# Kernel optimization log

Hardware: AMD Instinct MI355X
Metric: run time of the kernel (lower is better)

## Reference

```python
import jax, jax.numpy as jnp
import numpy as np

N = 50000      # nodes
R = 4          # relations
E = 1600000    # edges per relation
IN = 256       # in_feats
H = 256        # h_feats
C = 16         # num_classes


def setup_inputs() -> dict:
    key = jax.random.key(0)
    ks = jax.random.split(key, 8)
    X = jax.random.normal(ks[0], (N, IN), jnp.float32)
    edge_index = jax.random.randint(ks[1], (R, 2, E), 0, N, dtype=jnp.int32)
    W1 = jax.random.normal(ks[2], (R, IN, H), jnp.float32) * (1.0 / np.sqrt(IN))
    W2 = jax.random.normal(ks[3], (R, H, H), jnp.float32) * (1.0 / np.sqrt(H))
    att_q = jax.random.normal(ks[4], (H,), jnp.float32) * (1.0 / np.sqrt(H))
    tau = jnp.asarray(2.0, jnp.float32)
    W_out = jax.random.normal(ks[5], (H, C), jnp.float32) * (1.0 / np.sqrt(H))
    b_out = jnp.zeros((C,), jnp.float32)
    return {"X": X, "edge_index": edge_index, "W1": W1, "W2": W2,
            "att_q": att_q, "tau": tau, "W_out": W_out, "b_out": b_out}


def _sym_norm_spmm(edge, feat):
    """out = D^{-1/2} A D^{-1/2} @ feat for one relation, edge: [2,E]."""
    row, col = edge[0], edge[1]
    ones = jnp.ones(edge.shape[1], feat.dtype)
    deg_r = jax.ops.segment_sum(ones, row, num_segments=N)
    deg_c = jax.ops.segment_sum(ones, col, num_segments=N)
    dinv_r = jax.lax.rsqrt(jnp.maximum(deg_r, 1.0))
    dinv_c = jax.lax.rsqrt(jnp.maximum(deg_c, 1.0))
    w = dinv_r[row] * dinv_c[col]                      # [E]
    msg = w[:, None] * feat[col]                       # gather + scale
    return jax.ops.segment_sum(msg, row, num_segments=N)  # [N, F]


def _rel_layer(edge_index, feat, W):
    # vmapped over relations: ReLU(A_r feat W_r) -> [R, N, H]
    def one(edge, Wr):
        return jax.nn.relu(_sym_norm_spmm(edge, feat) @ Wr)
    return jax.vmap(one)(edge_index, W)


def reference(X, edge_index, W1, W2, att_q, tau, W_out, b_out):
    # Layer 1: mean over relations (eval mode: no dropout)
    H1 = _rel_layer(edge_index, X, W1)        # [R, N, H]
    h1 = H1.mean(axis=0)                      # [N, H]
    # Layer 2 with relation attention
    H2 = _rel_layer(edge_index, h1, W2)       # [R, N, H]
    scores = jnp.einsum('rnh,h->nr', H2, att_q)
    tau_c = jnp.clip(tau, 0.5, 5.0)
    alpha = jax.nn.softmax(scores / tau_c, axis=1)   # [N, R]
    h2_att = jnp.einsum('nr,rnh->nh', alpha, H2)
    h2 = H2.mean(axis=0) + h2_att             # residual fusion
    logits = h2 @ W_out + b_out               # [N, C]
    return logits, alpha
```

## Files before the change

### kernel.cpp

```cpp
#include <hip/hip_runtime.h>
#include <hip/hip_bf16.h>
#include <stdint.h>

#define NODES 50000
#define RELS  4
#define EDGES 1600000
#define FEAT  256
#define NCLS  16
#define MPAD  50048
#define RPS   50016
#define SCHUNK 1024
#define NSBLK  49
#define NCHUNK 64
#define CHUNKE 25000
#define NB     782

typedef __attribute__((ext_vector_type(8))) short short8;
typedef __attribute__((ext_vector_type(8))) unsigned short u16x8;
typedef __attribute__((ext_vector_type(4))) float f32x4;

static __device__ __forceinline__ float bf2f(unsigned short u) {
    return __uint_as_float(((unsigned int)u) << 16);
}
static __device__ __forceinline__ unsigned short f2bf(float f) {
    unsigned int x = __float_as_uint(f);
    unsigned int r = x + 0x7fffu + ((x >> 16) & 1u);
    return (unsigned short)(r >> 16);
}


__global__ __launch_bounds__(256)
void k_bhist2(const int* __restrict__ edges, unsigned* __restrict__ partR,
              unsigned* __restrict__ partC) {
    int chunk = blockIdx.x, rel = blockIdx.y, t = threadIdx.x;
    const int* rows = edges + (size_t)rel * 2 * EDGES + (size_t)chunk * CHUNKE;
    const int* cols = rows + EDGES;
    __shared__ unsigned hR[NB];
    __shared__ unsigned hC[NB];
    for (int i = t; i < NB; i += 256) { hR[i] = 0; hC[i] = 0; }
    __syncthreads();
    for (int e = t; e < CHUNKE; e += 256) {
        atomicAdd(&hR[((unsigned)rows[e]) >> 6], 1u);
        atomicAdd(&hC[((unsigned)cols[e]) >> 6], 1u);
    }
    __syncthreads();
    unsigned* pR = partR + ((size_t)rel * NCHUNK + chunk) * NB;
    unsigned* pC = partC + ((size_t)rel * NCHUNK + chunk) * NB;
    for (int i = t; i < NB; i += 256) { pR[i] = hR[i]; pC[i] = hC[i]; }
}

__global__ __launch_bounds__(256)
void k_bscan(const unsigned* __restrict__ part, unsigned* __restrict__ off,
             unsigned* __restrict__ bbase) {
    int rel = blockIdx.x, t = threadIdx.x;
    const int BPT = 4;
    int b0 = t * BPT;
    unsigned s = 0;
#pragma unroll
    for (int j = 0; j < BPT; ++j) {
        int b = b0 + j;
        unsigned x = 0;
        if (b < NB)
            for (int c = 0; c < NCHUNK; ++c)
                x += part[((size_t)rel * NCHUNK + c) * NB + b];
        s += x;
    }
    __shared__ unsigned sh[256];
    sh[t] = s;
    __syncthreads();
    for (int o = 1; o < 256; o <<= 1) {
        unsigned u = (t >= o) ? sh[t - o] : 0;
        __syncthreads();
        sh[t] += u;
        __syncthreads();
    }
    unsigned base = sh[t] - s;
#pragma unroll
    for (int j = 0; j < BPT; ++j) {
        int b = b0 + j;
        if (b < NB) {
            bbase[rel * (NB + 1) + b] = base;
            unsigned acc = base;
            for (int c = 0; c < NCHUNK; ++c) {
                size_t o2 = ((size_t)rel * NCHUNK + c) * NB + b;
                off[o2] = acc;
                acc += part[o2];
            }
            base = acc;
        }
    }
    if (t == 255) bbase[rel * (NB + 1) + NB] = sh[255];
}

__global__ __launch_bounds__(256)
void k_scat2(const int* __restrict__ edges, const unsigned* __restrict__ offR,
             const unsigned* __restrict__ offC, int2* __restrict__ ebuf,
             int* __restrict__ cbuf) {
    int chunk = blockIdx.x, rel = blockIdx.y, t = threadIdx.x;
    const int* rows = edges + (size_t)rel * 2 * EDGES + (size_t)chunk * CHUNKE;
    const int* cols = rows + EDGES;
    __shared__ unsigned curR[NB];
    __shared__ unsigned curC[NB];
    const unsigned* pR = offR + ((size_t)rel * NCHUNK + chunk) * NB;
    const unsigned* pC = offC + ((size_t)rel * NCHUNK + chunk) * NB;
    for (int i = t; i < NB; i += 256) { curR[i] = pR[i]; curC[i] = pC[i]; }
    __syncthreads();
    int2* eb = ebuf + (size_t)rel * EDGES;
    int*  cb = cbuf + (size_t)rel * EDGES;
    for (int e = t; e < CHUNKE; e += 256) {
        int r = rows[e], c = cols[e];
        unsigned pr = atomicAdd(&curR[((unsigned)r) >> 6], 1u);
        eb[pr] = make_int2(r, c);
        unsigned pc = atomicAdd(&curC[((unsigned)c) >> 6], 1u);
        cb[pc] = c;
    }
}

__global__ __launch_bounds__(256)
void k_countR(const int2* __restrict__ ebuf, const unsigned* __restrict__ bbase,
              int* __restrict__ deg_row) {
    int b = blockIdx.x, rel = blockIdx.y, t = threadIdx.x;
    unsigned s = bbase[rel * (NB + 1) + b], e = bbase[rel * (NB + 1) + b + 1];
    __shared__ unsigned cnt[64];
    if (t < 64) cnt[t] = 0;
    __syncthreads();
    const int2* eb = ebuf + (size_t)rel * EDGES;
    for (unsigned i = s + t; i < e; i += 256) atomicAdd(&cnt[eb[i].x & 63], 1u);
    __syncthreads();
    int base = b * 64;
    if (t < 64 && base + t < NODES) deg_row[(size_t)rel * NODES + base + t] = (int)cnt[t];
}

__global__ __launch_bounds__(256)
void k_countC(const int* __restrict__ cbuf, const unsigned* __restrict__ bbase,
              int* __restrict__ deg_col) {
    int b = blockIdx.x, rel = blockIdx.y, t = threadIdx.x;
    unsigned s = bbase[rel * (NB + 1) + b], e = bbase[rel * (NB + 1) + b + 1];
    __shared__ unsigned cnt[64];
    if (t < 64) cnt[t] = 0;
    __syncthreads();
    const int* cb = cbuf + (size_t)rel * EDGES;
    for (unsigned i = s + t; i < e; i += 256) atomicAdd(&cnt[cb[i] & 63], 1u);
    __syncthreads();
    int base = b * 64;
    if (t < 64 && base + t < NODES) deg_col[(size_t)rel * NODES + base + t] = (int)cnt[t];
}

__global__ void k_dinv(const int* __restrict__ deg_row, const int* __restrict__ deg_col,
                       float* dinv_row, float* dinv_col) {
    int idx = blockIdx.x * blockDim.x + threadIdx.x;
    if (idx >= RELS * NODES) return;
    int dr = deg_row[idx]; if (dr < 1) dr = 1;
    int dc = deg_col[idx]; if (dc < 1) dc = 1;
    dinv_row[idx] = rsqrtf((float)dr);
    dinv_col[idx] = rsqrtf((float)dc);
}

__global__ __launch_bounds__(256)
void k_scanA(const int* __restrict__ deg, int* __restrict__ tmp, int* __restrict__ btot) {
    int r = blockIdx.y, blk = blockIdx.x, t = threadIdx.x;
    int i0 = blk * SCHUNK + t * 4;
    const int* d = deg + (size_t)r * NODES;
    int4 v = make_int4(0, 0, 0, 0);
    if (i0 + 3 < NODES) v = *(const int4*)(d + i0);
    else if (i0 < NODES) {
        v.x = d[i0];
        if (i0 + 1 < NODES) v.y = d[i0 + 1];
        if (i0 + 2 < NODES) v.z = d[i0 + 2];
    }
    int s = v.x + v.y + v.z + v.w;
    __shared__ int sh[256];
    sh[t] = s;
    __syncthreads();
    for (int off = 1; off < 256; off <<= 1) {
        int u = (t >= off) ? sh[t - off] : 0;
        __syncthreads();
        sh[t] += u;
        __syncthreads();
    }
    int excl = sh[t] - s;
    int4 o;
    o.x = excl; o.y = excl + v.x; o.z = o.y + v.y; o.w = o.z + v.z;
    int* tp = tmp + (size_t)r * NODES;
    if (i0 + 3 < NODES) *(int4*)(tp + i0) = o;
    else if (i0 < NODES) {
        tp[i0] = o.x;
        if (i0 + 1 < NODES) tp[i0 + 1] = o.y;
        if (i0 + 2 < NODES) tp[i0 + 2] = o.z;
    }
    if (t == 255) btot[r * 64 + blk] = sh[255];
}

__global__ void k_scanB(int* __restrict__ btot, int* __restrict__ row_ptr) {
    int r = blockIdx.x;
    if (threadIdx.x != 0) return;
    int acc = 0;
    for (int b = 0; b < NSBLK; ++b) {
        int v = btot[r * 64 + b];
        btot[r * 64 + b] = acc;
        acc += v;
    }
    row_ptr[r * RPS + NODES] = acc;
}

__global__ __launch_bounds__(256)
void k_scanC(const int* __restrict__ tmp, const int* __restrict__ btot,
             int* __restrict__ row_ptr) {
    int r = blockIdx.y, blk = blockIdx.x, t = threadIdx.x;
    int i0 = blk * SCHUNK + t * 4;
    int off = btot[r * 64 + blk];
    const int* tp = tmp + (size_t)r * NODES;
    int* rp = row_ptr + (size_t)r * RPS;
    if (i0 + 3 < NODES) {
        int4 v = *(const int4*)(tp + i0);
        rp[i0] = v.x + off; rp[i0 + 1] = v.y + off;
        rp[i0 + 2] = v.z + off; rp[i0 + 3] = v.w + off;
    } else if (i0 < NODES) {
        for (int j = 0; j < 4 && i0 + j < NODES; ++j)
            rp[i0 + j] = tp[i0 + j] + off;
    }
}

__global__ __launch_bounds__(256)
void k_place(const int2* __restrict__ ebuf, const unsigned* __restrict__ bbase,
             const int* __restrict__ row_ptr, int* __restrict__ csr_col) {
    int b = blockIdx.x, rel = blockIdx.y, t = threadIdx.x;
    unsigned s = bbase[rel * (NB + 1) + b], e = bbase[rel * (NB + 1) + b + 1];
    __shared__ int cur[64];
    int base = b * 64;
    const int* rp = row_ptr + (size_t)rel * RPS;
    if (t < 64) cur[t] = (base + t < NODES) ? rp[base + t] : 0;
    __syncthreads();
    const int2* eb = ebuf + (size_t)rel * EDGES;
    int* cc = csr_col + (size_t)rel * EDGES;
    for (unsigned i = s + t; i < e; i += 256) {
        int2 ec = eb[i];
        int pos = atomicAdd(&cur[ec.x - base], 1);
        cc[pos] = ec.y;
    }
}


__global__ __launch_bounds__(256)
void k_f2bf8(const float* __restrict__ src, unsigned short* __restrict__ dst, int count8) {
    int i = blockIdx.x * 256 + threadIdx.x;
    if (i >= count8) return;
    const float* s = src + (size_t)i * 8;
    float4 a = *(const float4*)s;
    float4 b = *(const float4*)(s + 4);
    u16x8 v;
    v[0] = f2bf(a.x); v[1] = f2bf(a.y); v[2] = f2bf(a.z); v[3] = f2bf(a.w);
    v[4] = f2bf(b.x); v[5] = f2bf(b.y); v[6] = f2bf(b.z); v[7] = f2bf(b.w);
    *(u16x8*)(dst + (size_t)i * 8) = v;
}

__global__ void k_wt2(const float* __restrict__ W1, const float* __restrict__ W2,
                      unsigned short* __restrict__ W1t, unsigned short* __restrict__ W2t) {
    int idx = blockIdx.x * blockDim.x + threadIdx.x;
    const int half = RELS * FEAT * FEAT;
    if (idx >= 2 * half) return;
    const float* W = (idx < half) ? W1 : W2;
    unsigned short* Wt = (idx < half) ? W1t : W2t;
    int id = (idx < half) ? idx : idx - half;
    int r = id >> 16;
    int rem = id & 65535;
    int n = rem >> 8;
    int k = rem & 255;
    Wt[id] = f2bf(W[(size_t)r * FEAT * FEAT + (size_t)k * FEAT + n]);
}


__global__ __launch_bounds__(256)
void k_spmm(const unsigned short* __restrict__ feat, const int* __restrict__ row_ptr,
            const int* __restrict__ csr_col, const float* __restrict__ dinv_row,
            const float* __restrict__ dinv_col, unsigned short* __restrict__ aggbase,
            int slice_off) {
    int rel = blockIdx.y;
    unsigned short* aggbf = aggbase + (size_t)(rel + slice_off) * (size_t)MPAD * FEAT;
    int wave = (blockIdx.x * blockDim.x + threadIdx.x) >> 6;
    int lane = threadIdx.x & 63;
    if (wave >= NODES) return;
    int row = wave;
    int half = lane >> 5;
    int l32  = lane & 31;
    int start = row_ptr[rel * RPS + row];
    int end   = row_ptr[rel * RPS + row + 1];
    const int* cols = csr_col + (size_t)rel * EDGES;
    const float* dc = dinv_col + rel * NODES;
    const unsigned short* fb = feat + l32 * 8;
    float acc[8] = {0.f, 0.f, 0.f, 0.f, 0.f, 0.f, 0.f, 0.f};
    int j = start + half;
    for (; j + 2 < end; j += 4) {
        int c0 = cols[j];
        int c1 = cols[j + 2];
        float w0 = dc[c0];
        float w1 = dc[c1];
        u16x8 u0 = *(const u16x8*)(fb + (size_t)c0 * FEAT);
        u16x8 u1 = *(const u16x8*)(fb + (size_t)c1 * FEAT);
#pragma unroll
        for (int i = 0; i < 8; ++i) acc[i] += w0 * bf2f(u0[i]);
#pragma unroll
        for (int i = 0; i < 8; ++i) acc[i] += w1 * bf2f(u1[i]);
    }
    if (j < end) {
        int c0 = cols[j];
        float w0 = dc[c0];
        u16x8 u0 = *(const u16x8*)(fb + (size_t)c0 * FEAT);
#pragma unroll
        for (int i = 0; i < 8; ++i) acc[i] += w0 * bf2f(u0[i]);
    }
#pragma unroll
    for (int i = 0; i < 8; ++i) acc[i] += __shfl_down(acc[i], 32, 64);
    if (half == 0) {
        float dr = dinv_row[rel * NODES + row];
        u16x8 o;
#pragma unroll
        for (int i = 0; i < 8; ++i) o[i] = f2bf(acc[i] * dr);
        *(u16x8*)(aggbf + (size_t)row * FEAT + l32 * 8) = o;
    }
}


__global__ __launch_bounds__(256)
void k_gemm1(const unsigned short* __restrict__ Abase, const unsigned short* __restrict__ Wt,
             unsigned short* __restrict__ h1bf) {
    __shared__ __align__(16) unsigned short As[128 * 64];
    __shared__ __align__(16) unsigned short Bs[128 * 64];
    int tid = threadIdx.x;
    int wave = tid >> 6, lane = tid & 63;
    int quad = lane >> 4, l16 = lane & 15;
    int wm = (wave & 1) * 64, wn = (wave >> 1) * 64;
    int row0 = blockIdx.x * 128, n0 = blockIdx.y * 128;

    f32x4 hacc[4][4];
#pragma unroll
    for (int mi = 0; mi < 4; ++mi)
#pragma unroll
        for (int ni = 0; ni < 4; ++ni)
            hacc[mi][ni] = (f32x4){0.f, 0.f, 0.f, 0.f};

    for (int r = 0; r < RELS; ++r) {
        const unsigned short* A  = Abase + (size_t)r * MPAD * FEAT;
        const unsigned short* Bt = Wt + (size_t)r * FEAT * FEAT;
        f32x4 acc[4][4];
#pragma unroll
        for (int mi = 0; mi < 4; ++mi)
#pragma unroll
            for (int ni = 0; ni < 4; ++ni)
                acc[mi][ni] = (f32x4){0.f, 0.f, 0.f, 0.f};

        for (int k0 = 0; k0 < FEAT; k0 += 64) {
#pragma unroll
            for (int issue = 0; issue < 4; ++issue) {
                int flat = issue * 256 + tid;
                int row = flat >> 3;
                int gr = flat & 7;
                int sg = gr ^ (row & 7);
                *(uint4*)&As[flat * 8] = *(const uint4*)(A + (size_t)(row0 + row) * FEAT + k0 + sg * 8);
                *(uint4*)&Bs[flat * 8] = *(const uint4*)(Bt + (size_t)(n0 + row) * FEAT + k0 + sg * 8);
            }
            __syncthreads();
#pragma unroll
            for (int ks = 0; ks < 2; ++ks) {
                int g = ks * 4 + quad;
                short8 af[4], bfr[4];
#pragma unroll
                for (int mi = 0; mi < 4; ++mi) {
                    int m = wm + mi * 16 + l16;
                    af[mi] = *(const short8*)&As[m * 64 + ((g ^ (m & 7)) << 3)];
                }
#pragma unroll
                for (int ni = 0; ni < 4; ++ni) {
                    int n = wn + ni * 16 + l16;
                    bfr[ni] = *(const short8*)&Bs[n * 64 + ((g ^ (n & 7)) << 3)];
                }
#pragma unroll
                for (int mi = 0; mi < 4; ++mi)
#pragma unroll
                    for (int ni = 0; ni < 4; ++ni)
                        acc[mi][ni] = __builtin_amdgcn_mfma_f32_16x16x32_bf16(af[mi], bfr[ni], acc[mi][ni], 0, 0, 0);
            }
            __syncthreads();
        }
#pragma unroll
        for (int mi = 0; mi < 4; ++mi)
#pragma unroll
            for (int ni = 0; ni < 4; ++ni)
#pragma unroll
                for (int i = 0; i < 4; ++i) {
                    float v = acc[mi][ni][i];
                    hacc[mi][ni][i] += 0.25f * (v > 0.f ? v : 0.f);
                }
    }

#pragma unroll
    for (int mi = 0; mi < 4; ++mi)
#pragma unroll
        for (int ni = 0; ni < 4; ++ni) {
            int col = n0 + wn + ni * 16 + l16;
#pragma unroll
            for (int i = 0; i < 4; ++i) {
                int row = row0 + wm + mi * 16 + quad * 4 + i;
                if (row < NODES) h1bf[(size_t)row * FEAT + col] = f2bf(hacc[mi][ni][i]);
            }
        }
}

__global__ __launch_bounds__(256)
void k_gemm2z(const unsigned short* __restrict__ aggbase, const unsigned short* __restrict__ Wtb,
              unsigned short* __restrict__ o0, unsigned short* __restrict__ o1,
              unsigned short* __restrict__ o2, unsigned short* __restrict__ o3) {
    __shared__ __align__(16) unsigned short As[128 * 64];
    __shared__ __align__(16) unsigned short Bs[128 * 64];
    int rz = blockIdx.z;
    const unsigned short* A  = aggbase + (size_t)(rz + 1) * MPAD * FEAT;
    const unsigned short* Bt = Wtb + (size_t)rz * FEAT * FEAT;
    unsigned short* H2 = (rz == 0) ? o0 : (rz == 1) ? o1 : (rz == 2) ? o2 : o3;

    int tid = threadIdx.x;
    int wave = tid >> 6, lane = tid & 63;
    int quad = lane >> 4, l16 = lane & 15;
    int wm = (wave & 1) * 64, wn = (wave >> 1) * 64;
    int row0 = blockIdx.x * 128, n0 = blockIdx.y * 128;

    f32x4 acc[4][4];
#pragma unroll
    for (int mi = 0; mi < 4; ++mi)
#pragma unroll
        for (int ni = 0; ni < 4; ++ni)
            acc[mi][ni] = (f32x4){0.f, 0.f, 0.f, 0.f};

    for (int k0 = 0; k0 < FEAT; k0 += 64) {
#pragma unroll
        for (int issue = 0; issue < 4; ++issue) {
            int flat = issue * 256 + tid;
            int row = flat >> 3;
            int gr = flat & 7;
            int sg = gr ^ (row & 7);
            *(uint4*)&As[flat * 8] = *(const uint4*)(A + (size_t)(row0 + row) * FEAT + k0 + sg * 8);
            *(uint4*)&Bs[flat * 8] = *(const uint4*)(Bt + (size_t)(n0 + row) * FEAT + k0 + sg * 8);
        }
        __syncthreads();
#pragma unroll
        for (int ks = 0; ks < 2; ++ks) {
            int g = ks * 4 + quad;
            short8 af[4], bfr[4];
#pragma unroll
            for (int mi = 0; mi < 4; ++mi) {
                int m = wm + mi * 16 + l16;
                af[mi] = *(const short8*)&As[m * 64 + ((g ^ (m & 7)) << 3)];
            }
#pragma unroll
            for (int ni = 0; ni < 4; ++ni) {
                int n = wn + ni * 16 + l16;
                bfr[ni] = *(const short8*)&Bs[n * 64 + ((g ^ (n & 7)) << 3)];
            }
#pragma unroll
            for (int mi = 0; mi < 4; ++mi)
#pragma unroll
                for (int ni = 0; ni < 4; ++ni)
                    acc[mi][ni] = __builtin_amdgcn_mfma_f32_16x16x32_bf16(af[mi], bfr[ni], acc[mi][ni], 0, 0, 0);
        }
        __syncthreads();
    }

#pragma unroll
    for (int mi = 0; mi < 4; ++mi)
#pragma unroll
        for (int ni = 0; ni < 4; ++ni) {
            int col = n0 + wn + ni * 16 + l16;
#pragma unroll
            for (int i = 0; i < 4; ++i) {
                int row = row0 + wm + mi * 16 + quad * 4 + i;
                if (row < NODES) {
                    float v = acc[mi][ni][i];
                    H2[(size_t)row * FEAT + col] = f2bf(v > 0.f ? v : 0.f);
                }
            }
        }
}


__global__ __launch_bounds__(256)
void k_attn_out(const unsigned short* __restrict__ p0, const unsigned short* __restrict__ p1,
                const unsigned short* __restrict__ p2, const unsigned short* __restrict__ p3,
                const float* __restrict__ att_q, const float* __restrict__ tau_p,
                const float* __restrict__ W_out, const float* __restrict__ b_out,
                float* __restrict__ alpha_out, float* __restrict__ logits) {
    __shared__ float red[4][64 * 17];
    int tid = threadIdx.x;
    int wid = tid >> 6;
    int lane = tid & 63;
    int gwave = blockIdx.x * 4 + wid;
    int nwaves = gridDim.x * 4;

    const unsigned short* hp[RELS] = {p0, p1, p2, p3};
    float4 q = *(const float4*)(att_q + lane * 4);
    float tau = fminf(fmaxf(tau_p[0], 0.5f), 5.0f);
    float itau = 1.0f / tau;
    f32x4 Wr[4][4];
#pragma unroll
    for (int j = 0; j < 4; ++j)
#pragma unroll
        for (int c4 = 0; c4 < 4; ++c4) {
            float4 w = *(const float4*)(W_out + (size_t)(lane * 4 + j) * NCLS + c4 * 4);
            Wr[j][c4] = (f32x4){w.x, w.y, w.z, w.w};
        }
    float bc = b_out[lane & 15];
    float* myred = &red[wid][0];
    int cls = lane & 15;
    int rb = (lane >> 4) * 16;

    int n = gwave;
    if (n >= NODES) return;
    ushort4 u[RELS];
#pragma unroll
    for (int r = 0; r < RELS; ++r)
        u[r] = *(const ushort4*)(hp[r] + (size_t)n * FEAT + lane * 4);

    while (n < NODES) {
        int nn = n + nwaves;
        int nc = (nn < NODES) ? nn : n;
        ushort4 un[RELS];
#pragma unroll
        for (int r = 0; r < RELS; ++r)
            un[r] = *(const ushort4*)(hp[r] + (size_t)nc * FEAT + lane * 4);

        float h[RELS][4];
#pragma unroll
        for (int r = 0; r < RELS; ++r) {
            h[r][0] = bf2f(u[r].x); h[r][1] = bf2f(u[r].y);
            h[r][2] = bf2f(u[r].z); h[r][3] = bf2f(u[r].w);
        }
        float s[RELS];
#pragma unroll
        for (int r = 0; r < RELS; ++r)
            s[r] = h[r][0] * q.x + h[r][1] * q.y + h[r][2] * q.z + h[r][3] * q.w;
#pragma unroll
        for (int off = 1; off < 64; off <<= 1) {
#pragma unroll
            for (int r = 0; r < RELS; ++r) s[r] += __shfl_xor(s[r], off, 64);
        }
        float m = fmaxf(fmaxf(s[0], s[1]), fmaxf(s[2], s[3]));
        float e[RELS];
        float esum = 0.f;
#pragma unroll
        for (int r = 0; r < RELS; ++r) { e[r] = expf((s[r] - m) * itau); esum += e[r]; }
        float inv = 1.0f / esum;
        float a[RELS];
#pragma unroll
        for (int r = 0; r < RELS; ++r) a[r] = e[r] * inv;
        if (lane == 0)
            *(float4*)(alpha_out + (size_t)n * 4) = make_float4(a[0], a[1], a[2], a[3]);

        float w0 = 0.25f + a[0], w1 = 0.25f + a[1], w2 = 0.25f + a[2], w3 = 0.25f + a[3];
        float h2[4];
#pragma unroll
        for (int j = 0; j < 4; ++j)
            h2[j] = w0 * h[0][j] + w1 * h[1][j] + w2 * h[2][j] + w3 * h[3][j];

        f32x4 acc[4];
#pragma unroll
        for (int c4 = 0; c4 < 4; ++c4)
            acc[c4] = h2[0] * Wr[0][c4] + h2[1] * Wr[1][c4]
                    + h2[2] * Wr[2][c4] + h2[3] * Wr[3][c4];

#pragma unroll
        for (int c4 = 0; c4 < 4; ++c4)
#pragma unroll
            for (int i = 0; i < 4; ++i)
                myred[lane * 17 + c4 * 4 + i] = acc[c4][i];
        asm volatile("s_waitcnt lgkmcnt(0)" ::: "memory");
        float t = 0.f;
#pragma unroll
        for (int k = 0; k < 16; ++k) t += myred[(rb + k) * 17 + cls];
        t += __shfl_xor(t, 16, 64);
        t += __shfl_xor(t, 32, 64);
        if (lane < 16) logits[(size_t)n * NCLS + lane] = t + bc;
        asm volatile("" ::: "memory");

#pragma unroll
        for (int r = 0; r < RELS; ++r) u[r] = un[r];
        n = nn;
    }
}


static inline int cdiv(int a, int b) { return (a + b - 1) / b; }

extern "C" void kernel_launch(void* const* d_in, const int* in_sizes, int n_in,
                              void* d_out, int out_size, void* d_ws, size_t ws_size,
                              hipStream_t stream) {
    const float* X     = (const float*)d_in[0];
    const int*   edges = (const int*)d_in[1];
    const float* W1    = (const float*)d_in[2];
    const float* W2    = (const float*)d_in[3];
    const float* att_q = (const float*)d_in[4];
    const float* tau   = (const float*)d_in[5];
    const float* W_out = (const float*)d_in[6];
    const float* b_out = (const float*)d_in[7];

    float* logits = (float*)d_out;
    float* alpha  = logits + (size_t)NODES * NCLS;

    char* p = (char*)d_ws;
    auto carve = [&](size_t bytes) -> char* {
        char* q = p;
        p += (bytes + 255) & ~(size_t)255;
        return q;
    };
    int*   deg_row  = (int*)carve((size_t)RELS * NODES * 4);
    int*   deg_col  = (int*)carve((size_t)RELS * NODES * 4);
    float* dinv_row = (float*)carve((size_t)RELS * NODES * 4);
    float* dinv_col = (float*)carve((size_t)RELS * NODES * 4);
    int*   row_ptr  = (int*)carve((size_t)RELS * RPS * 4 + 256);
    int*   tmp      = (int*)carve((size_t)RELS * NODES * 4);
    int*   btot     = (int*)carve((size_t)RELS * 64 * 4);
    int*   csr_col  = (int*)carve((size_t)RELS * EDGES * 4);
    unsigned short* Xbf  = (unsigned short*)carve((size_t)NODES * FEAT * 2);
    unsigned short* h1bf = (unsigned short*)carve((size_t)NODES * FEAT * 2);
    unsigned short* W1t  = (unsigned short*)carve((size_t)RELS * FEAT * FEAT * 2);
    unsigned short* W2t  = (unsigned short*)carve((size_t)RELS * FEAT * FEAT * 2);
    const size_t AGGSE = (size_t)MPAD * FEAT;
    char* BIG = carve(5 * AGGSE * 2);
    int2*     ebuf = (int2*)BIG;
    int*      cbuf = (int*)(BIG + (size_t)RELS * EDGES * 8);
    char*     q = BIG + (size_t)RELS * EDGES * 12;
    unsigned* partR = (unsigned*)q;               q += (size_t)RELS * NCHUNK * NB * 4;
    unsigned* offR  = (unsigned*)q;               q += (size_t)RELS * NCHUNK * NB * 4;
    unsigned* partC = (unsigned*)q;               q += (size_t)RELS * NCHUNK * NB * 4;
    unsigned* offC  = (unsigned*)q;               q += (size_t)RELS * NCHUNK * NB * 4;
    unsigned* bbR   = (unsigned*)q;               q += (size_t)RELS * (NB + 1) * 4;
    unsigned* bbC   = (unsigned*)q;
    unsigned short* aggbf = (unsigned short*)BIG;
    unsigned short* H2_0 = aggbf;
    unsigned short* H2_1 = Xbf;
    unsigned short* H2_2 = h1bf;
    unsigned short* H2_3 = (unsigned short*)csr_col;

    {
        dim3 hg(NCHUNK, RELS);
        dim3 bg(NB, RELS);
        k_bhist2<<<hg, 256, 0, stream>>>(edges, partR, partC);
        k_bscan<<<RELS, 256, 0, stream>>>(partR, offR, bbR);
        k_bscan<<<RELS, 256, 0, stream>>>(partC, offC, bbC);
        k_scat2<<<hg, 256, 0, stream>>>(edges, offR, offC, ebuf, cbuf);
        k_countR<<<bg, 256, 0, stream>>>(ebuf, bbR, deg_row);
        k_countC<<<bg, 256, 0, stream>>>(cbuf, bbC, deg_col);
        k_dinv<<<cdiv(RELS * NODES, 256), 256, 0, stream>>>(deg_row, deg_col, dinv_row, dinv_col);
        dim3 sg(NSBLK, RELS);
        k_scanA<<<sg, 256, 0, stream>>>(deg_row, tmp, btot);
        k_scanB<<<RELS, 64, 0, stream>>>(btot, row_ptr);
        k_scanC<<<sg, 256, 0, stream>>>(tmp, btot, row_ptr);
        k_place<<<bg, 256, 0, stream>>>(ebuf, bbR, row_ptr, csr_col);
    }

    k_wt2<<<cdiv(2 * RELS * FEAT * FEAT, 256), 256, 0, stream>>>(W1, W2, W1t, W2t);
    k_f2bf8<<<cdiv(NODES * FEAT / 8, 256), 256, 0, stream>>>(X, Xbf, NODES * FEAT / 8);

    dim3 gemm_grid(MPAD / 128, FEAT / 128);
    dim3 gemm2_grid(MPAD / 128, FEAT / 128, RELS);
    dim3 spmm_grid(cdiv(NODES * 64, 256), RELS);

    k_spmm<<<spmm_grid, 256, 0, stream>>>(Xbf, row_ptr, csr_col, dinv_row, dinv_col,
                                          aggbf, 0);
    k_gemm1<<<gemm_grid, 256, 0, stream>>>(aggbf, W1t, h1bf);

    k_spmm<<<spmm_grid, 256, 0, stream>>>(h1bf, row_ptr, csr_col, dinv_row, dinv_col,
                                          aggbf, 1);
    k_gemm2z<<<gemm2_grid, 256, 0, stream>>>(aggbf, W2t, H2_0, H2_1, H2_2, H2_3);

    k_attn_out<<<1024, 256, 0, stream>>>(H2_0, H2_1, H2_2, H2_3, att_q, tau,
                                         W_out, b_out, alpha, logits);
}
```

Baseline: 1.458 ms.

## Fuse row counting, scan and CSR placement into one bucket kernel with packed edges

```diff
diff --git a/kernel.cpp b/kernel.cpp
--- a/kernel.cpp
+++ b/kernel.cpp
@@ -9,8 +9,6 @@
 #define NCLS  16
 #define MPAD  50048
 #define RPS   50016
-#define SCHUNK 1024
-#define NSBLK  49
 #define NCHUNK 64
 #define CHUNKE 25000
 #define NB     782
@@ -94,7 +92,7 @@
 
 __global__ __launch_bounds__(256)
 void k_scat2(const int* __restrict__ edges, const unsigned* __restrict__ offR,
-             const unsigned* __restrict__ offC, int2* __restrict__ ebuf,
+             const unsigned* __restrict__ offC, unsigned* __restrict__ ebuf,
              int* __restrict__ cbuf) {
     int chunk = blockIdx.x, rel = blockIdx.y, t = threadIdx.x;
     const int* rows = edges + (size_t)rel * 2 * EDGES + (size_t)chunk * CHUNKE;
@@ -105,138 +103,72 @@
     const unsigned* pC = offC + ((size_t)rel * NCHUNK + chunk) * NB;
     for (int i = t; i < NB; i += 256) { curR[i] = pR[i]; curC[i] = pC[i]; }
     __syncthreads();
-    int2* eb = ebuf + (size_t)rel * EDGES;
-    int*  cb = cbuf + (size_t)rel * EDGES;
+    unsigned* eb = ebuf + (size_t)rel * EDGES;
+    int*      cb = cbuf + (size_t)rel * EDGES;
     for (int e = t; e < CHUNKE; e += 256) {
         int r = rows[e], c = cols[e];
         unsigned pr = atomicAdd(&curR[((unsigned)r) >> 6], 1u);
-        eb[pr] = make_int2(r, c);
+        eb[pr] = (((unsigned)(r & 63)) << 16) | (unsigned)c;
         unsigned pc = atomicAdd(&curC[((unsigned)c) >> 6], 1u);
         cb[pc] = c;
     }
 }
 
 __global__ __launch_bounds__(256)
-void k_countR(const int2* __restrict__ ebuf, const unsigned* __restrict__ bbase,
-              int* __restrict__ deg_row) {
+void k_countC(const int* __restrict__ cbuf, const unsigned* __restrict__ bbase,
+              float* __restrict__ dinv_col) {
     int b = blockIdx.x, rel = blockIdx.y, t = threadIdx.x;
     unsigned s = bbase[rel * (NB + 1) + b], e = bbase[rel * (NB + 1) + b + 1];
     __shared__ unsigned cnt[64];
     if (t < 64) cnt[t] = 0;
     __syncthreads();
-    const int2* eb = ebuf + (size_t)rel * EDGES;
-    for (unsigned i = s + t; i < e; i += 256) atomicAdd(&cnt[eb[i].x & 63], 1u);
+    const int* cb = cbuf + (size_t)rel * EDGES;
+    for (unsigned i = s + t; i < e; i += 256) atomicAdd(&cnt[cb[i] & 63], 1u);
     __syncthreads();
     int base = b * 64;
-    if (t < 64 && base + t < NODES) deg_row[(size_t)rel * NODES + base + t] = (int)cnt[t];
-}
-
-__global__ __launch_bounds__(256)
-void k_countC(const int* __restrict__ cbuf, const unsigned* __restrict__ bbase,
-              int* __restrict__ deg_col) {
+    if (t < 64 && base + t < NODES) {
+        int d = (int)cnt[t]; if (d < 1) d = 1;
+        dinv_col[(size_t)rel * NODES + base + t] = rsqrtf((float)d);
+    }
+}
+
+__global__ __launch_bounds__(256)
+void k_place2(const unsigned* __restrict__ ebuf, const unsigned* __restrict__ bbase,
+              int* __restrict__ csr_col, int* __restrict__ row_ptr,
+              float* __restrict__ dinv_row) {
     int b = blockIdx.x, rel = blockIdx.y, t = threadIdx.x;
     unsigned s = bbase[rel * (NB + 1) + b], e = bbase[rel * (NB + 1) + b + 1];
     __shared__ unsigned cnt[64];
+    __shared__ int cur[64];
     if (t < 64) cnt[t] = 0;
     __syncthreads();
-    const int* cb = cbuf + (size_t)rel * EDGES;
-    for (unsigned i = s + t; i < e; i += 256) atomicAdd(&cnt[cb[i] & 63], 1u);
-    __syncthreads();
-    int base = b * 64;
-    if (t < 64 && base + t < NODES) deg_col[(size_t)rel * NODES + base + t] = (int)cnt[t];
-}
-
-__global__ void k_dinv(const int* __restrict__ deg_row, const int* __restrict__ deg_col,
-                       float* dinv_row, float* dinv_col) {
-    int idx = blockIdx.x * blockDim.x + threadIdx.x;
-    if (idx >= RELS * NODES) return;
-    int dr = deg_row[idx]; if (dr < 1) dr = 1;
-    int dc = deg_col[idx]; if (dc < 1) dc = 1;
-    dinv_row[idx] = rsqrtf((float)dr);
-    dinv_col[idx] = rsqrtf((float)dc);
-}
-
-__global__ __launch_bounds__(256)
-void k_scanA(const int* __restrict__ deg, int* __restrict__ tmp, int* __restrict__ btot) {
-    int r = blockIdx.y, blk = blockIdx.x, t = threadIdx.x;
-    int i0 = blk * SCHUNK + t * 4;
-    const int* d = deg + (size_t)r * NODES;
-    int4 v = make_int4(0, 0, 0, 0);
-    if (i0 + 3 < NODES) v = *(const int4*)(d + i0);
-    else if (i0 < NODES) {
-        v.x = d[i0];
-        if (i0 + 1 < NODES) v.y = d[i0 + 1];
-        if (i0 + 2 < NODES) v.z = d[i0 + 2];
-    }
-    int s = v.x + v.y + v.z + v.w;
-    __shared__ int sh[256];
-    sh[t] = s;
-    __syncthreads();
-    for (int off = 1; off < 256; off <<= 1) {
-        int u = (t >= off) ? sh[t - off] : 0;
-        __syncthreads();
-        sh[t] += u;
-        __syncthreads();
-    }
-    int excl = sh[t] - s;
-    int4 o;
-    o.x = excl; o.y = excl + v.x; o.z = o.y + v.y; o.w = o.z + v.z;
-    int* tp = tmp + (size_t)r * NODES;
-    if (i0 + 3 < NODES) *(int4*)(tp + i0) = o;
-    else if (i0 < NODES) {
-        tp[i0] = o.x;
-        if (i0 + 1 < NODES) tp[i0 + 1] = o.y;
-        if (i0 + 2 < NODES) tp[i0 + 2] = o.z;
-    }
-    if (t == 255) btot[r * 64 + blk] = sh[255];
-}
-
-__global__ void k_scanB(int* __restrict__ btot, int* __restrict__ row_ptr) {
-    int r = blockIdx.x;
-    if (threadIdx.x != 0) return;
-    int acc = 0;
-    for (int b = 0; b < NSBLK; ++b) {
-        int v = btot[r * 64 + b];
-        btot[r * 64 + b] = acc;
-        acc += v;
-    }
-    row_ptr[r * RPS + NODES] = acc;
-}
-
-__global__ __launch_bounds__(256)
-void k_scanC(const int* __restrict__ tmp, const int* __restrict__ btot,
-             int* __restrict__ row_ptr) {
-    int r = blockIdx.y, blk = blockIdx.x, t = threadIdx.x;
-    int i0 = blk * SCHUNK + t * 4;
-    int off = btot[r * 64 + blk];
-    const int* tp = tmp + (size_t)r * NODES;
-    int* rp = row_ptr + (size_t)r * RPS;
-    if (i0 + 3 < NODES) {
-        int4 v = *(const int4*)(tp + i0);
-        rp[i0] = v.x + off; rp[i0 + 1] = v.y + off;
-        rp[i0 + 2] = v.z + off; rp[i0 + 3] = v.w + off;
-    } else if (i0 < NODES) {
-        for (int j = 0; j < 4 && i0 + j < NODES; ++j)
-            rp[i0 + j] = tp[i0 + j] + off;
-    }
-}
-
-__global__ __launch_bounds__(256)
-void k_place(const int2* __restrict__ ebuf, const unsigned* __restrict__ bbase,
-             const int* __restrict__ row_ptr, int* __restrict__ csr_col) {
-    int b = blockIdx.x, rel = blockIdx.y, t = threadIdx.x;
-    unsigned s = bbase[rel * (NB + 1) + b], e = bbase[rel * (NB + 1) + b + 1];
-    __shared__ int cur[64];
-    int base = b * 64;
-    const int* rp = row_ptr + (size_t)rel * RPS;
-    if (t < 64) cur[t] = (base + t < NODES) ? rp[base + t] : 0;
-    __syncthreads();
-    const int2* eb = ebuf + (size_t)rel * EDGES;
+    const unsigned* eb = ebuf + (size_t)rel * EDGES;
+    for (unsigned i = s + t; i < e; i += 256) atomicAdd(&cnt[eb[i] >> 16], 1u);
+    __syncthreads();
+    if (t < 64) {
+        unsigned c = cnt[t];
+        unsigned v = c;
+#pragma unroll
+        for (int off = 1; off < 64; off <<= 1) {
+            unsigned n = __shfl_up(v, off, 64);
+            if (t >= off) v += n;
+        }
+        unsigned excl = v - c;
+        int base = b * 64;
+        cur[t] = (int)(s + excl);
+        if (base + t < NODES) {
+            row_ptr[rel * RPS + base + t] = (int)(s + excl);
+            int d = (int)c; if (d < 1) d = 1;
+            dinv_row[(size_t)rel * NODES + base + t] = rsqrtf((float)d);
+        }
+        if (b == 0 && t == 0) row_ptr[rel * RPS + NODES] = EDGES;
+    }
+    __syncthreads();
     int* cc = csr_col + (size_t)rel * EDGES;
     for (unsigned i = s + t; i < e; i += 256) {
-        int2 ec = eb[i];
-        int pos = atomicAdd(&cur[ec.x - base], 1);
-        cc[pos] = ec.y;
+        unsigned v = eb[i];
+        int pos = atomicAdd(&cur[v >> 16], 1);
+        cc[pos] = (int)(v & 0xFFFFu);
     }
 }
 
@@ -609,13 +541,9 @@
         p += (bytes + 255) & ~(size_t)255;
         return q;
     };
-    int*   deg_row  = (int*)carve((size_t)RELS * NODES * 4);
-    int*   deg_col  = (int*)carve((size_t)RELS * NODES * 4);
     float* dinv_row = (float*)carve((size_t)RELS * NODES * 4);
     float* dinv_col = (float*)carve((size_t)RELS * NODES * 4);
     int*   row_ptr  = (int*)carve((size_t)RELS * RPS * 4 + 256);
-    int*   tmp      = (int*)carve((size_t)RELS * NODES * 4);
-    int*   btot     = (int*)carve((size_t)RELS * 64 * 4);
     int*   csr_col  = (int*)carve((size_t)RELS * EDGES * 4);
     unsigned short* Xbf  = (unsigned short*)carve((size_t)NODES * FEAT * 2);
     unsigned short* h1bf = (unsigned short*)carve((size_t)NODES * FEAT * 2);
@@ -623,9 +551,9 @@
     unsigned short* W2t  = (unsigned short*)carve((size_t)RELS * FEAT * FEAT * 2);
     const size_t AGGSE = (size_t)MPAD * FEAT;
     char* BIG = carve(5 * AGGSE * 2);
-    int2*     ebuf = (int2*)BIG;
-    int*      cbuf = (int*)(BIG + (size_t)RELS * EDGES * 8);
-    char*     q = BIG + (size_t)RELS * EDGES * 12;
+    unsigned* ebuf = (unsigned*)BIG;
+    int*      cbuf = (int*)(BIG + (size_t)RELS * EDGES * 4);
+    char*     q = BIG + (size_t)RELS * EDGES * 8;
     unsigned* partR = (unsigned*)q;               q += (size_t)RELS * NCHUNK * NB * 4;
     unsigned* offR  = (unsigned*)q;               q += (size_t)RELS * NCHUNK * NB * 4;
     unsigned* partC = (unsigned*)q;               q += (size_t)RELS * NCHUNK * NB * 4;
@@ -645,14 +573,8 @@
         k_bscan<<<RELS, 256, 0, stream>>>(partR, offR, bbR);
         k_bscan<<<RELS, 256, 0, stream>>>(partC, offC, bbC);
         k_scat2<<<hg, 256, 0, stream>>>(edges, offR, offC, ebuf, cbuf);
-        k_countR<<<bg, 256, 0, stream>>>(ebuf, bbR, deg_row);
-        k_countC<<<bg, 256, 0, stream>>>(cbuf, bbC, deg_col);
-        k_dinv<<<cdiv(RELS * NODES, 256), 256, 0, stream>>>(deg_row, deg_col, dinv_row, dinv_col);
-        dim3 sg(NSBLK, RELS);
-        k_scanA<<<sg, 256, 0, stream>>>(deg_row, tmp, btot);
-        k_scanB<<<RELS, 64, 0, stream>>>(btot, row_ptr);
-        k_scanC<<<sg, 256, 0, stream>>>(tmp, btot, row_ptr);
-        k_place<<<bg, 256, 0, stream>>>(ebuf, bbR, row_ptr, csr_col);
+        k_countC<<<bg, 256, 0, stream>>>(cbuf, bbC, dinv_col);
+        k_place2<<<bg, 256, 0, stream>>>(ebuf, bbR, csr_col, row_ptr, dinv_row);
     }
 
     k_wt2<<<cdiv(2 * RELS * FEAT * FEAT, 256), 256, 0, stream>>>(W1, W2, W1t, W2t);
```

Measured after the change: 1.437 ms. About the same (-1.4%).
